# Performance work log

Measured on AMD Instinct MI355X. Metric: run time of the kernel, lower is better.

## Reference

```python
import jax, jax.numpy as jnp
import numpy as np

N_NODES = 50000
N_EDGES = 800000
IN_FEATS = 128
HIDDEN = 128
NUM_CLASSES = 47


def setup_inputs() -> dict:
    key = jax.random.key(0)
    k1, k2, k3, k4 = jax.random.split(key, 4)
    features = jax.random.normal(k1, (N_NODES, IN_FEATS), dtype=jnp.float32)
    edge_index = jax.random.randint(k2, (2, N_EDGES), 0, N_NODES, dtype=jnp.int32)
    # Glorot-style init for weights, zeros for bias (DGL GraphConv defaults)
    W1 = jax.random.normal(k3, (IN_FEATS, HIDDEN), dtype=jnp.float32) * (1.0 / np.sqrt(IN_FEATS))
    b1 = jnp.zeros((HIDDEN,), dtype=jnp.float32)
    W2 = jax.random.normal(k4, (HIDDEN, NUM_CLASSES), dtype=jnp.float32) * (1.0 / np.sqrt(HIDDEN))
    b2 = jnp.zeros((NUM_CLASSES,), dtype=jnp.float32)
    return {"features": features, "edge_index": edge_index,
            "W1": W1, "b1": b1, "W2": W2, "b2": b2}


def _graph_conv(x, W, b, src, dst, norm_src, norm_dst, n_nodes):
    # DGL GraphConv, norm='both': D_dst^{-1/2} A D_src^{-1/2} (X W) + b
    h = (x * norm_src[:, None]) @ W            # transform before aggregation
    agg = jax.ops.segment_sum(h[src], dst, num_segments=n_nodes)
    return agg * norm_dst[:, None] + b


def reference(features, edge_index, W1, b1, W2, b2):
    src, dst = edge_index[0], edge_index[1]
    n = features.shape[0]
    ones = jnp.ones((src.shape[0],), dtype=features.dtype)
    deg_out = jax.ops.segment_sum(ones, src, num_segments=n)
    deg_in = jax.ops.segment_sum(ones, dst, num_segments=n)
    norm_src = jax.lax.rsqrt(jnp.clip(deg_out, 1.0))   # d_out^{-1/2}, clamp >= 1
    norm_dst = jax.lax.rsqrt(jnp.clip(deg_in, 1.0))    # d_in^{-1/2}, clamp >= 1

    h = _graph_conv(features, W1, b1, src, dst, norm_src, norm_dst, n)
    h = jax.nn.relu(h)
    out = _graph_conv(h, W2, b2, src, dst, norm_src, norm_dst, n)
    return out
```

## Files before the change

### kernel.cpp

```cpp
#include <hip/hip_runtime.h>
#include <hip/hip_fp16.h>

#define N_NODES 50000
#define N_EDGES 800000
#define IN_F 128
#define HID 128
#define NCLS 47
#define H2S 48
#define W2C 64
#define NCH 196
#define TM 32
#define XTS 40
#define NB 64
#define CHUNK 12500
#define PDW 12500
#define HHALF 6250
#define FQ 3125
#define NHIST 256
#define FG_LDS 20480


struct __align__(8)  h2x2 { __half2 a, b; };
struct __align__(16) h2x4 { __half2 a, b, c, d; };

__global__ __launch_bounds__(512) void hist_kernel(const int* __restrict__ ei,
                                                   unsigned int* __restrict__ Pdst,
                                                   unsigned int* __restrict__ Psrc) {
    __shared__ unsigned int h[HHALF];
    const int t = threadIdx.x;
    const int job = blockIdx.x;
    const bool is_src = job >= NHIST / 2;
    const int half = (job >> 6) & 1;
    const int chunk = job & (NB - 1);
    const int* ids = is_src ? ei : ei + N_EDGES;
    uint2* h2 = (uint2*)h;
    for (int j = t; j < HHALF / 2; j += 512) h2[j] = make_uint2(0u, 0u);
    __syncthreads();
    const int e0 = chunk * CHUNK;
    const int lo = half * HHALF;
    for (int k = t; k < CHUNK; k += 512) {
        int v = ids[e0 + k];
        int rel = (v >> 2) - lo;
        if ((unsigned)rel < HHALF)
            atomicAdd(&h[rel], 1u << ((v & 3) * 8));
    }
    __syncthreads();
    unsigned int* P = (is_src ? Psrc : Pdst) + (size_t)chunk * PDW + lo;
    uint2* P2 = (uint2*)P;
    for (int j = t; j < HHALF / 2; j += 512) P2[j] = h2[j];
}

__global__ __launch_bounds__(256) void reduce_kernel(unsigned int* __restrict__ Pdst,
                                                     const unsigned int* __restrict__ Psrc,
                                                     int* __restrict__ cnt_in,
                                                     float* __restrict__ norm_src,
                                                     float* __restrict__ norm_dst,
                                                     int* __restrict__ chunk_sums) {
    __shared__ int sm[256];
    const int t = threadIdx.x;
    const int j = blockIdx.x * 256 + t;
    int tot = 0;
    if (j < PDW) {
        unsigned int run = 0;
        for (int b = 0; b < NB; ++b) {
            unsigned int v = Pdst[(size_t)b * PDW + j];
            Pdst[(size_t)b * PDW + j] = run;
            run += v;
        }
        int n0 = run & 0xff, n1 = (run >> 8) & 0xff;
        int n2 = (run >> 16) & 0xff, n3 = (run >> 24) & 0xff;
        *(int4*)&cnt_in[4 * j] = make_int4(n0, n1, n2, n3);
        *(float4*)&norm_dst[4 * j] = make_float4(
            rsqrtf(fmaxf((float)n0, 1.0f)), rsqrtf(fmaxf((float)n1, 1.0f)),
            rsqrtf(fmaxf((float)n2, 1.0f)), rsqrtf(fmaxf((float)n3, 1.0f)));
        tot = n0 + n1 + n2 + n3;
        unsigned int rs = 0;
        for (int b = 0; b < NB; ++b) rs += Psrc[(size_t)b * PDW + j];
        int s0 = rs & 0xff, s1 = (rs >> 8) & 0xff;
        int s2 = (rs >> 16) & 0xff, s3 = (rs >> 24) & 0xff;
        *(float4*)&norm_src[4 * j] = make_float4(
            rsqrtf(fmaxf((float)s0, 1.0f)), rsqrtf(fmaxf((float)s1, 1.0f)),
            rsqrtf(fmaxf((float)s2, 1.0f)), rsqrtf(fmaxf((float)s3, 1.0f)));
    }
    sm[t] = tot;
    __syncthreads();
    const int g = t & 63;
    for (int off = 32; off > 0; off >>= 1) {
        if (g < off) sm[t] += sm[t + off];
        __syncthreads();
    }
    if (g == 0) chunk_sums[blockIdx.x * 4 + (t >> 6)] = sm[t];
}

__global__ __launch_bounds__(256) void scan3_kernel(const int* __restrict__ cnt_in,
                                                    const int* __restrict__ chunk_sums,
                                                    int* __restrict__ offsets,
                                                    const float* __restrict__ W2,
                                                    float* __restrict__ W2p) {
    __shared__ int sm[256];
    const int t = threadIdx.x;
    int v = (t < NCH) ? chunk_sums[t] : 0;
    sm[t] = v;
    __syncthreads();
    for (int off = 1; off < 256; off <<= 1) {
        int u = (t >= off) ? sm[t - off] : 0;
        __syncthreads();
        sm[t] += u;
        __syncthreads();
    }
    const int basev = (blockIdx.x == 0) ? 0 : sm[blockIdx.x - 1];
    __syncthreads();
    const int idx = blockIdx.x * 256 + t;
    int c = (idx < N_NODES) ? cnt_in[idx] : 0;
    sm[t] = c;
    __syncthreads();
    for (int off = 1; off < 256; off <<= 1) {
        int u = (t >= off) ? sm[t - off] : 0;
        __syncthreads();
        sm[t] += u;
        __syncthreads();
    }
    if (idx < N_NODES) offsets[idx] = basev + sm[t] - c;
    if (blockIdx.x == 0) {
        if (t == 0) offsets[N_NODES] = N_EDGES;
        for (int i2 = t; i2 < HID * W2C; i2 += 256) {
            int k = i2 >> 6, cc = i2 & 63;
            W2p[i2] = (cc < NCLS) ? W2[k * NCLS + cc] : 0.f;
        }
    }
}

__global__ __launch_bounds__(256) void fill_gemm1_kernel(const int* __restrict__ src,
        const int* __restrict__ dst, const int* __restrict__ offsets,
        const unsigned int* __restrict__ Pdst, int* __restrict__ csr_src,
        const float* __restrict__ X, const float* __restrict__ W1,
        __half* __restrict__ H1h) {
    __shared__ __align__(16) char smem[FG_LDS];
    const int t = threadIdx.x;
    if (blockIdx.x < 4 * NB) {
        unsigned int* cur = (unsigned int*)smem;
        const int quarter = blockIdx.x >> 6;
        const int chunk = blockIdx.x & (NB - 1);
        for (int j = t; j < FQ; j += 256) cur[j] = 0u;
        __syncthreads();
        const unsigned int* base = Pdst + (size_t)chunk * PDW;
        const int e0 = chunk * CHUNK;
        const int lo = quarter * FQ;
        for (int k = t; k < CHUNK; k += 256) {
            int d = dst[e0 + k];
            int rel = (d >> 2) - lo;
            if ((unsigned)rel < FQ) {
                const int sh = (d & 3) * 8;
                unsigned int old = atomicAdd(&cur[rel], 1u << sh);
                unsigned int rank = (old >> sh) & 0xffu;
                unsigned int bh = (base[d >> 2] >> sh) & 0xffu;
                csr_src[offsets[d] + (int)bh + (int)rank] = src[e0 + k];
            }
        }
    } else {
        float* xs = (float*)smem;
        const int row0 = (blockIdx.x - 4 * NB) * TM;
#pragma unroll
        for (int i = 0; i < 4; ++i) {
            int id = t + 256 * i;
            int r = id & 31;
            int q = id >> 5;
            int row = row0 + r;
            float4 v = make_float4(0.f, 0.f, 0.f, 0.f);
            if (row < N_NODES) v = *(const float4*)&X[(size_t)row * IN_F + 4 * q];
            xs[(4 * q + 0) * XTS + r] = v.x;
            xs[(4 * q + 1) * XTS + r] = v.y;
            xs[(4 * q + 2) * XTS + r] = v.z;
            xs[(4 * q + 3) * XTS + r] = v.w;
        }
        __syncthreads();
        const int c = t & 31;
        const int rg = t >> 5;
        float acc[4][4] = {{0.f}};
#pragma unroll 4
        for (int k = 0; k < IN_F; ++k) {
            const float4 w4 = *(const float4*)&W1[k * HID + 4 * c];
            const float4 a4 = *(const float4*)&xs[k * XTS + 4 * rg];
            const float wv[4] = {w4.x, w4.y, w4.z, w4.w};
            const float av[4] = {a4.x, a4.y, a4.z, a4.w};
#pragma unroll
            for (int i = 0; i < 4; ++i)
#pragma unroll
                for (int j = 0; j < 4; ++j)
                    acc[i][j] += av[i] * wv[j];
        }
#pragma unroll
        for (int i = 0; i < 4; ++i) {
            int row = row0 + 4 * rg + i;
            if (row < N_NODES) {
                h2x2 p = {__floats2half2_rn(acc[i][0], acc[i][1]),
                          __floats2half2_rn(acc[i][2], acc[i][3])};
                *(h2x2*)&H1h[(size_t)row * HID + 4 * c] = p;
            }
        }
    }
}

__global__ __launch_bounds__(256) void gather1_kernel(const __half* __restrict__ H1h,
        const int* __restrict__ offsets, const int* __restrict__ csr_src,
        const float* __restrict__ b1, const float* __restrict__ norm_src,
        const float* __restrict__ norm_dst, __half* __restrict__ Hrelu16) {
    const int lane = threadIdx.x & 63;
    const int q = lane >> 4;
    const int fl = lane & 15;
    const int row = blockIdx.x * 4 + (threadIdx.x >> 6);
    const int beg = offsets[row], end = offsets[row + 1];
    float a0 = 0.f, a1 = 0.f, a2 = 0.f, a3 = 0.f;
    float a4 = 0.f, a5 = 0.f, a6 = 0.f, a7 = 0.f;
    for (int base = beg; base < end; base += 64) {
        int idx = 0;
        float nsv = 0.f;
        if (base + lane < end) {
            idx = csr_src[base + lane];
            nsv = norm_src[idx];
        }
        const int cnt = min(end - base, 64);
        for (int j = 0; j < cnt; j += 16) {
            int e0 = j + q, e1 = j + 4 + q, e2 = j + 8 + q, e3 = j + 12 + q;
            int s0 = __shfl(idx, e0);  float n0 = __shfl(nsv, e0);
            int s1 = __shfl(idx, e1);  float n1 = __shfl(nsv, e1);
            int s2 = __shfl(idx, e2);  float n2 = __shfl(nsv, e2);
            int s3 = __shfl(idx, e3);  float n3 = __shfl(nsv, e3);
            h2x4 v0 = *(const h2x4*)&H1h[(size_t)s0 * HID + 8 * fl];
            h2x4 v1 = *(const h2x4*)&H1h[(size_t)s1 * HID + 8 * fl];
            h2x4 v2 = *(const h2x4*)&H1h[(size_t)s2 * HID + 8 * fl];
            h2x4 v3 = *(const h2x4*)&H1h[(size_t)s3 * HID + 8 * fl];
            float2 f;
            f = __half22float2(v0.a); a0 = fmaf(f.x, n0, a0); a1 = fmaf(f.y, n0, a1);
            f = __half22float2(v0.b); a2 = fmaf(f.x, n0, a2); a3 = fmaf(f.y, n0, a3);
            f = __half22float2(v0.c); a4 = fmaf(f.x, n0, a4); a5 = fmaf(f.y, n0, a5);
            f = __half22float2(v0.d); a6 = fmaf(f.x, n0, a6); a7 = fmaf(f.y, n0, a7);
            f = __half22float2(v1.a); a0 = fmaf(f.x, n1, a0); a1 = fmaf(f.y, n1, a1);
            f = __half22float2(v1.b); a2 = fmaf(f.x, n1, a2); a3 = fmaf(f.y, n1, a3);
            f = __half22float2(v1.c); a4 = fmaf(f.x, n1, a4); a5 = fmaf(f.y, n1, a5);
            f = __half22float2(v1.d); a6 = fmaf(f.x, n1, a6); a7 = fmaf(f.y, n1, a7);
            f = __half22float2(v2.a); a0 = fmaf(f.x, n2, a0); a1 = fmaf(f.y, n2, a1);
            f = __half22float2(v2.b); a2 = fmaf(f.x, n2, a2); a3 = fmaf(f.y, n2, a3);
            f = __half22float2(v2.c); a4 = fmaf(f.x, n2, a4); a5 = fmaf(f.y, n2, a5);
            f = __half22float2(v2.d); a6 = fmaf(f.x, n2, a6); a7 = fmaf(f.y, n2, a7);
            f = __half22float2(v3.a); a0 = fmaf(f.x, n3, a0); a1 = fmaf(f.y, n3, a1);
            f = __half22float2(v3.b); a2 = fmaf(f.x, n3, a2); a3 = fmaf(f.y, n3, a3);
            f = __half22float2(v3.c); a4 = fmaf(f.x, n3, a4); a5 = fmaf(f.y, n3, a5);
            f = __half22float2(v3.d); a6 = fmaf(f.x, n3, a6); a7 = fmaf(f.y, n3, a7);
        }
    }
    a0 += __shfl_xor(a0, 16); a1 += __shfl_xor(a1, 16);
    a2 += __shfl_xor(a2, 16); a3 += __shfl_xor(a3, 16);
    a4 += __shfl_xor(a4, 16); a5 += __shfl_xor(a5, 16);
    a6 += __shfl_xor(a6, 16); a7 += __shfl_xor(a7, 16);
    a0 += __shfl_xor(a0, 32); a1 += __shfl_xor(a1, 32);
    a2 += __shfl_xor(a2, 32); a3 += __shfl_xor(a3, 32);
    a4 += __shfl_xor(a4, 32); a5 += __shfl_xor(a5, 32);
    a6 += __shfl_xor(a6, 32); a7 += __shfl_xor(a7, 32);
    if (lane < 16) {
        float nd = norm_dst[row], ns = norm_src[row];
        float4 bA = *(const float4*)&b1[8 * fl];
        float4 bB = *(const float4*)&b1[8 * fl + 4];
        float o0 = fmaxf(fmaf(a0, nd, bA.x), 0.f) * ns;
        float o1 = fmaxf(fmaf(a1, nd, bA.y), 0.f) * ns;
        float o2 = fmaxf(fmaf(a2, nd, bA.z), 0.f) * ns;
        float o3 = fmaxf(fmaf(a3, nd, bA.w), 0.f) * ns;
        float o4 = fmaxf(fmaf(a4, nd, bB.x), 0.f) * ns;
        float o5 = fmaxf(fmaf(a5, nd, bB.y), 0.f) * ns;
        float o6 = fmaxf(fmaf(a6, nd, bB.z), 0.f) * ns;
        float o7 = fmaxf(fmaf(a7, nd, bB.w), 0.f) * ns;
        h2x4 p = {__floats2half2_rn(o0, o1), __floats2half2_rn(o2, o3),
                  __floats2half2_rn(o4, o5), __floats2half2_rn(o6, o7)};
        *(h2x4*)&Hrelu16[(size_t)row * HID + 8 * fl] = p;
    }
}

__global__ __launch_bounds__(128) void gemm2_kernel(const __half* __restrict__ Hrelu16,
                                                    const float* __restrict__ W2p,
                                                    __half* __restrict__ H2h) {
    __shared__ __align__(16) float xs[HID * XTS];
    const int t = threadIdx.x;
    const int row0 = blockIdx.x * TM;
#pragma unroll
    for (int i = 0; i < 4; ++i) {
        int id = t + 128 * i;
        int r = id & 31;
        int g = id >> 5;
        int row = row0 + r;
        h2x4 v{};
        if (row < N_NODES) v = *(const h2x4*)&Hrelu16[(size_t)row * HID + 8 * g];
        float2 f0 = __half22float2(v.a), f1 = __half22float2(v.b);
        float2 f2 = __half22float2(v.c), f3 = __half22float2(v.d);
        xs[(8 * g + 0) * XTS + r] = f0.x;
        xs[(8 * g + 1) * XTS + r] = f0.y;
        xs[(8 * g + 2) * XTS + r] = f1.x;
        xs[(8 * g + 3) * XTS + r] = f1.y;
        xs[(8 * g + 4) * XTS + r] = f2.x;
        xs[(8 * g + 5) * XTS + r] = f2.y;
        xs[(8 * g + 6) * XTS + r] = f3.x;
        xs[(8 * g + 7) * XTS + r] = f3.y;
    }
    __syncthreads();
    const int c = t & 15;
    const int rg = t >> 4;
    float acc[4][4] = {{0.f}};
#pragma unroll 4
    for (int k = 0; k < HID; ++k) {
        const float4 w4 = *(const float4*)&W2p[k * W2C + 4 * c];
        const float4 a4 = *(const float4*)&xs[k * XTS + 4 * rg];
        const float wv[4] = {w4.x, w4.y, w4.z, w4.w};
        const float av[4] = {a4.x, a4.y, a4.z, a4.w};
#pragma unroll
        for (int i = 0; i < 4; ++i)
#pragma unroll
            for (int j = 0; j < 4; ++j)
                acc[i][j] += av[i] * wv[j];
    }
    if (c < 12) {
#pragma unroll
        for (int i = 0; i < 4; ++i) {
            int row = row0 + 4 * rg + i;
            if (row < N_NODES) {
                h2x2 p = {__floats2half2_rn(acc[i][0], acc[i][1]),
                          __floats2half2_rn(acc[i][2], acc[i][3])};
                *(h2x2*)&H2h[(size_t)row * H2S + 4 * c] = p;
            }
        }
    }
}

__global__ __launch_bounds__(256) void gather2_kernel(const __half* __restrict__ H2h,
        const int* __restrict__ offsets, const int* __restrict__ csr_src,
        const float* __restrict__ b2, const float* __restrict__ norm_dst,
        float* __restrict__ out) {
    const int lane = threadIdx.x & 63;
    const int row = blockIdx.x * 4 + (threadIdx.x >> 6);
    const int beg = offsets[row], end = offsets[row + 1];
    const int cl = min(lane, H2S - 1);
    float acc = 0.f;
    for (int base = beg; base < end; base += 64) {
        int idx = 0;
        float wv = 0.f;
        if (base + lane < end) {
            idx = csr_src[base + lane];
            wv = 1.f;
        }
        const int cnt = min(end - base, 64);
        for (int j = 0; j < cnt; j += 4) {
            int s0 = __shfl(idx, j);     float w0 = __shfl(wv, j);
            int s1 = __shfl(idx, j + 1); float w1 = __shfl(wv, j + 1);
            int s2 = __shfl(idx, j + 2); float w2 = __shfl(wv, j + 2);
            int s3 = __shfl(idx, j + 3); float w3 = __shfl(wv, j + 3);
            float f0 = __half2float(H2h[(size_t)s0 * H2S + cl]);
            float f1 = __half2float(H2h[(size_t)s1 * H2S + cl]);
            float f2 = __half2float(H2h[(size_t)s2 * H2S + cl]);
            float f3 = __half2float(H2h[(size_t)s3 * H2S + cl]);
            acc = fmaf(f0, w0, acc);
            acc = fmaf(f1, w1, acc);
            acc = fmaf(f2, w2, acc);
            acc = fmaf(f3, w3, acc);
        }
    }
    if (lane < NCLS) out[(size_t)row * NCLS + lane] = acc * norm_dst[row] + b2[lane];
}

extern "C" void kernel_launch(void* const* d_in, const int* in_sizes, int n_in,
                              void* d_out, int out_size, void* d_ws, size_t ws_size,
                              hipStream_t stream) {
    const float* X  = (const float*)d_in[0];
    const int*   ei = (const int*)d_in[1];
    const float* W1 = (const float*)d_in[2];
    const float* b1 = (const float*)d_in[3];
    const float* W2 = (const float*)d_in[4];
    const float* b2 = (const float*)d_in[5];
    float* out = (float*)d_out;

    const int* src = ei;
    const int* dst = ei + N_EDGES;

    char* w = (char*)d_ws;
    auto alloc = [&](size_t bytes) {
        char* p = w;
        w += (bytes + 255) & ~(size_t)255;
        return p;
    };
    float*  norm_src   = (float*)alloc(N_NODES * 4);
    float*  norm_dst   = (float*)alloc(N_NODES * 4);
    int*    cnt_in     = (int*)alloc(N_NODES * 4);
    int*    offsets    = (int*)alloc((N_NODES + 1) * 4);
    int*    csr_src    = (int*)alloc((size_t)N_EDGES * 4);
    int*    chunk_sums = (int*)alloc(NCH * 4);
    float*  W2p        = (float*)alloc((size_t)HID * W2C * 4);
    __half* H1h        = (__half*)alloc((size_t)N_NODES * HID * 2);
    __half* Hrelu16    = (__half*)alloc((size_t)N_NODES * HID * 2);
    __half* H2h        = (__half*)alloc((size_t)N_NODES * H2S * 2);
    unsigned int* Pdst = (unsigned int*)alloc((size_t)NB * PDW * 4);
    unsigned int* Psrc = (unsigned int*)alloc((size_t)NB * PDW * 4);

    const int gemm_blocks = (N_NODES + TM - 1) / TM;
    hist_kernel<<<NHIST, 512, 0, stream>>>(ei, Pdst, Psrc);
    reduce_kernel<<<(PDW + 255) / 256, 256, 0, stream>>>(Pdst, Psrc, cnt_in,
                                                         norm_src, norm_dst, chunk_sums);
    scan3_kernel<<<NCH, 256, 0, stream>>>(cnt_in, chunk_sums, offsets, W2, W2p);
    fill_gemm1_kernel<<<4 * NB + gemm_blocks, 256, 0, stream>>>(src, dst, offsets,
                                                                Pdst, csr_src,
                                                                X, W1, H1h);
    gather1_kernel<<<N_NODES / 4, 256, 0, stream>>>(H1h, offsets, csr_src, b1,
                                                    norm_src, norm_dst, Hrelu16);
    gemm2_kernel<<<gemm_blocks, 128, 0, stream>>>(Hrelu16, W2p, H2h);
    gather2_kernel<<<N_NODES / 4, 256, 0, stream>>>(H2h, offsets, csr_src, b2,
                                                    norm_dst, out);
}
```

Baseline: 219.4 us.

## Replace FP32 SIMT GEMMs with split-fp16 MFMA matrix-core GEMMs

Both dense transforms (X·W1 and Hrelu·W2) move from scalar FP32 FMA loops with LDS staging to MFMA 16x16x32 fp16 instructions. Precision is kept close to FP32 by splitting operands into high and low fp16 parts: three MFMAs per tile for GEMM1 and two for GEMM2, where the activations are already fp16. Transposed hi/lo weight copies are built once in the scan kernel. This cuts the compute cost of the GEMMs and removes the LDS transposes, at the price of scalar fp16 output stores and uncoalesced direct global loads of A fragments.

```diff
diff --git a/kernel.cpp b/kernel.cpp
--- a/kernel.cpp
+++ b/kernel.cpp
@@ -9,16 +9,17 @@
 #define H2S 48
 #define W2C 64
 #define NCH 196
-#define TM 32
-#define XTS 40
 #define NB 64
 #define CHUNK 12500
 #define PDW 12500
 #define HHALF 6250
 #define FQ 3125
 #define NHIST 256
-#define FG_LDS 20480
-
+#define GROWS 128
+
+
+typedef _Float16 f16x8 __attribute__((ext_vector_type(8)));
+typedef float f32x4 __attribute__((ext_vector_type(4)));
 
 struct __align__(8)  h2x2 { __half2 a, b; };
 struct __align__(16) h2x4 { __half2 a, b, c, d; };
@@ -95,8 +96,12 @@
 __global__ __launch_bounds__(256) void scan3_kernel(const int* __restrict__ cnt_in,
                                                     const int* __restrict__ chunk_sums,
                                                     int* __restrict__ offsets,
+                                                    const float* __restrict__ W1,
                                                     const float* __restrict__ W2,
-                                                    float* __restrict__ W2p) {
+                                                    __half* __restrict__ W1Th,
+                                                    __half* __restrict__ W1Tl,
+                                                    __half* __restrict__ W2Th,
+                                                    __half* __restrict__ W2Tl) {
     __shared__ int sm[256];
     const int t = threadIdx.x;
     int v = (t < NCH) ? chunk_sums[t] : 0;
@@ -123,9 +128,21 @@
     if (idx < N_NODES) offsets[idx] = basev + sm[t] - c;
     if (blockIdx.x == 0) {
         if (t == 0) offsets[N_NODES] = N_EDGES;
-        for (int i2 = t; i2 < HID * W2C; i2 += 256) {
-            int k = i2 >> 6, cc = i2 & 63;
-            W2p[i2] = (cc < NCLS) ? W2[k * NCLS + cc] : 0.f;
+        for (int i2 = t; i2 < W2C * HID; i2 += 256) {
+            int cc = i2 >> 7, k = i2 & 127;
+            float w = (cc < NCLS) ? W2[k * NCLS + cc] : 0.f;
+            __half h = __float2half_rn(w);
+            W2Th[i2] = h;
+            W2Tl[i2] = __float2half_rn(w - __half2float(h));
+        }
+    }
+    if (blockIdx.x == 1) {
+        for (int i2 = t; i2 < IN_F * HID; i2 += 256) {
+            int cc = i2 >> 7, k = i2 & 127;
+            float w = W1[k * HID + cc];
+            __half h = __float2half_rn(w);
+            W1Th[i2] = h;
+            W1Tl[i2] = __float2half_rn(w - __half2float(h));
         }
     }
 }
@@ -133,12 +150,11 @@
 __global__ __launch_bounds__(256) void fill_gemm1_kernel(const int* __restrict__ src,
         const int* __restrict__ dst, const int* __restrict__ offsets,
         const unsigned int* __restrict__ Pdst, int* __restrict__ csr_src,
-        const float* __restrict__ X, const float* __restrict__ W1,
-        __half* __restrict__ H1h) {
-    __shared__ __align__(16) char smem[FG_LDS];
+        const float* __restrict__ X, const __half* __restrict__ W1Th,
+        const __half* __restrict__ W1Tl, __half* __restrict__ H1h) {
+    __shared__ __align__(16) unsigned int cur[FQ];
     const int t = threadIdx.x;
     if (blockIdx.x < 4 * NB) {
-        unsigned int* cur = (unsigned int*)smem;
         const int quarter = blockIdx.x >> 6;
         const int chunk = blockIdx.x & (NB - 1);
         for (int j = t; j < FQ; j += 256) cur[j] = 0u;
@@ -158,46 +174,58 @@
             }
         }
     } else {
-        float* xs = (float*)smem;
-        const int row0 = (blockIdx.x - 4 * NB) * TM;
-#pragma unroll
-        for (int i = 0; i < 4; ++i) {
-            int id = t + 256 * i;
-            int r = id & 31;
-            int q = id >> 5;
-            int row = row0 + r;
-            float4 v = make_float4(0.f, 0.f, 0.f, 0.f);
-            if (row < N_NODES) v = *(const float4*)&X[(size_t)row * IN_F + 4 * q];
-            xs[(4 * q + 0) * XTS + r] = v.x;
-            xs[(4 * q + 1) * XTS + r] = v.y;
-            xs[(4 * q + 2) * XTS + r] = v.z;
-            xs[(4 * q + 3) * XTS + r] = v.w;
-        }
-        __syncthreads();
-        const int c = t & 31;
-        const int rg = t >> 5;
-        float acc[4][4] = {{0.f}};
-#pragma unroll 4
-        for (int k = 0; k < IN_F; ++k) {
-            const float4 w4 = *(const float4*)&W1[k * HID + 4 * c];
-            const float4 a4 = *(const float4*)&xs[k * XTS + 4 * rg];
-            const float wv[4] = {w4.x, w4.y, w4.z, w4.w};
-            const float av[4] = {a4.x, a4.y, a4.z, a4.w};
-#pragma unroll
-            for (int i = 0; i < 4; ++i)
-#pragma unroll
-                for (int j = 0; j < 4; ++j)
-                    acc[i][j] += av[i] * wv[j];
-        }
-#pragma unroll
-        for (int i = 0; i < 4; ++i) {
-            int row = row0 + 4 * rg + i;
-            if (row < N_NODES) {
-                h2x2 p = {__floats2half2_rn(acc[i][0], acc[i][1]),
-                          __floats2half2_rn(acc[i][2], acc[i][3])};
-                *(h2x2*)&H1h[(size_t)row * HID + 4 * c] = p;
-            }
-        }
+        const int lane = t & 63;
+        const int wv = t >> 6;
+        const int r16 = lane & 15;
+        const int kg = lane >> 4;
+        const int row0 = (blockIdx.x - 4 * NB) * GROWS + wv * 32;
+        f32x4 acc[2][8] = {};
+#pragma unroll
+        for (int s = 0; s < 4; ++s) {
+            const int k0 = 32 * s + 8 * kg;
+            f16x8 ah[2], al[2];
+#pragma unroll
+            for (int rt = 0; rt < 2; ++rt) {
+                int row = row0 + rt * 16 + r16;
+                int rc = row < N_NODES ? row : N_NODES - 1;
+                const float4 x0 = *(const float4*)&X[(size_t)rc * IN_F + k0];
+                const float4 x1 = *(const float4*)&X[(size_t)rc * IN_F + k0 + 4];
+                const float xv[8] = {x0.x, x0.y, x0.z, x0.w,
+                                     x1.x, x1.y, x1.z, x1.w};
+#pragma unroll
+                for (int j = 0; j < 8; ++j) {
+                    _Float16 h = (_Float16)xv[j];
+                    ah[rt][j] = h;
+                    al[rt][j] = (_Float16)(xv[j] - (float)h);
+                }
+            }
+#pragma unroll
+            for (int tt = 0; tt < 8; ++tt) {
+                const f16x8 bh = *(const f16x8*)&W1Th[(16 * tt + r16) * IN_F + k0];
+                const f16x8 bl = *(const f16x8*)&W1Tl[(16 * tt + r16) * IN_F + k0];
+#pragma unroll
+                for (int rt = 0; rt < 2; ++rt) {
+                    acc[rt][tt] = __builtin_amdgcn_mfma_f32_16x16x32_f16(
+                        ah[rt], bh, acc[rt][tt], 0, 0, 0);
+                    acc[rt][tt] = __builtin_amdgcn_mfma_f32_16x16x32_f16(
+                        al[rt], bh, acc[rt][tt], 0, 0, 0);
+                    acc[rt][tt] = __builtin_amdgcn_mfma_f32_16x16x32_f16(
+                        ah[rt], bl, acc[rt][tt], 0, 0, 0);
+                }
+            }
+        }
+#pragma unroll
+        for (int rt = 0; rt < 2; ++rt)
+#pragma unroll
+            for (int j = 0; j < 4; ++j) {
+                const int row = row0 + rt * 16 + 4 * kg + j;
+                if (row < N_NODES) {
+#pragma unroll
+                    for (int tt = 0; tt < 8; ++tt)
+                        H1h[(size_t)row * HID + 16 * tt + r16] =
+                            __float2half_rn(acc[rt][tt][j]);
+                }
+            }
     }
 }
 
@@ -275,58 +303,51 @@
     }
 }
 
-__global__ __launch_bounds__(128) void gemm2_kernel(const __half* __restrict__ Hrelu16,
-                                                    const float* __restrict__ W2p,
+__global__ __launch_bounds__(256) void gemm2_kernel(const __half* __restrict__ Hrelu16,
+                                                    const __half* __restrict__ W2Th,
+                                                    const __half* __restrict__ W2Tl,
                                                     __half* __restrict__ H2h) {
-    __shared__ __align__(16) float xs[HID * XTS];
-    const int t = threadIdx.x;
-    const int row0 = blockIdx.x * TM;
-#pragma unroll
-    for (int i = 0; i < 4; ++i) {
-        int id = t + 128 * i;
-        int r = id & 31;
-        int g = id >> 5;
-        int row = row0 + r;
-        h2x4 v{};
-        if (row < N_NODES) v = *(const h2x4*)&Hrelu16[(size_t)row * HID + 8 * g];
-        float2 f0 = __half22float2(v.a), f1 = __half22float2(v.b);
-        float2 f2 = __half22float2(v.c), f3 = __half22float2(v.d);
-        xs[(8 * g + 0) * XTS + r] = f0.x;
-        xs[(8 * g + 1) * XTS + r] = f0.y;
-        xs[(8 * g + 2) * XTS + r] = f1.x;
-        xs[(8 * g + 3) * XTS + r] = f1.y;
-        xs[(8 * g + 4) * XTS + r] = f2.x;
-        xs[(8 * g + 5) * XTS + r] = f2.y;
-        xs[(8 * g + 6) * XTS + r] = f3.x;
-        xs[(8 * g + 7) * XTS + r] = f3.y;
-    }
-    __syncthreads();
-    const int c = t & 15;
-    const int rg = t >> 4;
-    float acc[4][4] = {{0.f}};
-#pragma unroll 4
-    for (int k = 0; k < HID; ++k) {
-        const float4 w4 = *(const float4*)&W2p[k * W2C + 4 * c];
-        const float4 a4 = *(const float4*)&xs[k * XTS + 4 * rg];
-        const float wv[4] = {w4.x, w4.y, w4.z, w4.w};
-        const float av[4] = {a4.x, a4.y, a4.z, a4.w};
-#pragma unroll
-        for (int i = 0; i < 4; ++i)
-#pragma unroll
-            for (int j = 0; j < 4; ++j)
-                acc[i][j] += av[i] * wv[j];
-    }
-    if (c < 12) {
-#pragma unroll
-        for (int i = 0; i < 4; ++i) {
-            int row = row0 + 4 * rg + i;
+    const int lane = threadIdx.x & 63;
+    const int wv = threadIdx.x >> 6;
+    const int r16 = lane & 15;
+    const int kg = lane >> 4;
+    const int row0 = blockIdx.x * GROWS + wv * 32;
+    f32x4 acc[2][3] = {};
+#pragma unroll
+    for (int s = 0; s < 4; ++s) {
+        const int k0 = 32 * s + 8 * kg;
+        f16x8 a[2];
+#pragma unroll
+        for (int rt = 0; rt < 2; ++rt) {
+            int row = row0 + rt * 16 + r16;
+            int rc = row < N_NODES ? row : N_NODES - 1;
+            a[rt] = *(const f16x8*)&Hrelu16[(size_t)rc * HID + k0];
+        }
+#pragma unroll
+        for (int tt = 0; tt < 3; ++tt) {
+            const f16x8 bh = *(const f16x8*)&W2Th[(16 * tt + r16) * HID + k0];
+            const f16x8 bl = *(const f16x8*)&W2Tl[(16 * tt + r16) * HID + k0];
+#pragma unroll
+            for (int rt = 0; rt < 2; ++rt) {
+                acc[rt][tt] = __builtin_amdgcn_mfma_f32_16x16x32_f16(
+                    a[rt], bh, acc[rt][tt], 0, 0, 0);
+                acc[rt][tt] = __builtin_amdgcn_mfma_f32_16x16x32_f16(
+                    a[rt], bl, acc[rt][tt], 0, 0, 0);
+            }
+        }
+    }
+#pragma unroll
+    for (int rt = 0; rt < 2; ++rt)
+#pragma unroll
+        for (int j = 0; j < 4; ++j) {
+            const int row = row0 + rt * 16 + 4 * kg + j;
             if (row < N_NODES) {
-                h2x2 p = {__floats2half2_rn(acc[i][0], acc[i][1]),
-                          __floats2half2_rn(acc[i][2], acc[i][3])};
-                *(h2x2*)&H2h[(size_t)row * H2S + 4 * c] = p;
-            }
-        }
-    }
+#pragma unroll
+                for (int tt = 0; tt < 3; ++tt)
+                    H2h[(size_t)row * H2S + 16 * tt + r16] =
+                        __float2half_rn(acc[rt][tt][j]);
+            }
+        }
 }
 
 __global__ __launch_bounds__(256) void gather2_kernel(const __half* __restrict__ H2h,
@@ -390,24 +411,28 @@
     int*    offsets    = (int*)alloc((N_NODES + 1) * 4);
     int*    csr_src    = (int*)alloc((size_t)N_EDGES * 4);
     int*    chunk_sums = (int*)alloc(NCH * 4);
-    float*  W2p        = (float*)alloc((size_t)HID * W2C * 4);
+    __half* W1Th       = (__half*)alloc((size_t)IN_F * HID * 2);
+    __half* W1Tl       = (__half*)alloc((size_t)IN_F * HID * 2);
+    __half* W2Th       = (__half*)alloc((size_t)W2C * HID * 2);
+    __half* W2Tl       = (__half*)alloc((size_t)W2C * HID * 2);
     __half* H1h        = (__half*)alloc((size_t)N_NODES * HID * 2);
     __half* Hrelu16    = (__half*)alloc((size_t)N_NODES * HID * 2);
     __half* H2h        = (__half*)alloc((size_t)N_NODES * H2S * 2);
     unsigned int* Pdst = (unsigned int*)alloc((size_t)NB * PDW * 4);
     unsigned int* Psrc = (unsigned int*)alloc((size_t)NB * PDW * 4);
 
-    const int gemm_blocks = (N_NODES + TM - 1) / TM;
+    const int gemm_blocks = (N_NODES + GROWS - 1) / GROWS;
     hist_kernel<<<NHIST, 512, 0, stream>>>(ei, Pdst, Psrc);
     reduce_kernel<<<(PDW + 255) / 256, 256, 0, stream>>>(Pdst, Psrc, cnt_in,
                                                          norm_src, norm_dst, chunk_sums);
-    scan3_kernel<<<NCH, 256, 0, stream>>>(cnt_in, chunk_sums, offsets, W2, W2p);
+    scan3_kernel<<<NCH, 256, 0, stream>>>(cnt_in, chunk_sums, offsets,
+                                          W1, W2, W1Th, W1Tl, W2Th, W2Tl);
     fill_gemm1_kernel<<<4 * NB + gemm_blocks, 256, 0, stream>>>(src, dst, offsets,
                                                                 Pdst, csr_src,
-                                                                X, W1, H1h);
+                                                                X, W1Th, W1Tl, H1h);
     gather1_kernel<<<N_NODES / 4, 256, 0, stream>>>(H1h, offsets, csr_src, b1,
                                                     norm_src, norm_dst, Hrelu16);
-    gemm2_kernel<<<gemm_blocks, 128, 0, stream>>>(Hrelu16, W2p, H2h);
+    gemm2_kernel<<<gemm_blocks, 256, 0, stream>>>(Hrelu16, W2Th, W2Tl, H2h);
     gather2_kernel<<<N_NODES / 4, 256, 0, stream>>>(H2h, offsets, csr_src, b2,
                                                     norm_dst, out);
 }
```

Result: faster. 204.6 us (-6.7%).
